# Kernel optimization log

Hardware: AMD Instinct MI355X
Metric: run time of the kernel (lower is better)

The kernel has to match this reference:

```python
import jax, jax.numpy as jnp
import numpy as np
import math

B, S, D, H = 4, 512, 1024, 16
DH = D // H
DQ = D // 4
MIN_STEPS, MAX_STEPS = 4, 12
THR = 1e-4


def lin(t, w, b):
    # torch Linear convention: w is (out, in)
    return jnp.einsum('...i,oi->...o', t, w) + b


def gelu(t):
    return jax.nn.gelu(t, approximate=False)  # torch nn.GELU() exact


def layernorm(t, g, b):
    m = t.mean(-1, keepdims=True)
    v = jnp.mean(jnp.square(t - m), axis=-1, keepdims=True)
    return (t - m) * jax.lax.rsqrt(v + 1e-5) * g + b


def _forward(h, x, ig_w1, ig_b1, ig_w2, ig_b2, wq, bq, wk, bk, wv, bv, wo, bo,
             g1_w1, g1_b1, g1_w2, g1_b2, gate_logits, ln_g, ln_b,
             sp_w1, sp_b1, sp_w2, sp_b2):
    # adaptive step count: steps = base + floor(sigmoid(MLP(mean_pool(h))).mean() * extra)
    pooled = h.mean(axis=1)  # (B, D)
    extra = jax.nn.sigmoid(lin(gelu(lin(pooled, sp_w1, sp_b1)), sp_w2, sp_b2)).mean()
    num_steps = jnp.minimum(
        MIN_STEPS + jnp.floor(extra * (MAX_STEPS - MIN_STEPS)).astype(jnp.int32), MAX_STEPS)

    gw = jax.nn.softmax(gate_logits)  # gate weights over the 3 gates
    scale = 1.0 / math.sqrt(DH)

    def step(carry, i):
        h, active = carry
        # G1 gate (G2/G3 multiply zero memory/expert outputs -> drop)
        G1 = jax.nn.sigmoid(lin(gelu(lin(h, g1_w1, g1_b1)), g1_w2, g1_b2)) * gw[0]
        # Phi: input-gated blend + raw multi-head self-attention
        gate = jax.nn.sigmoid(
            lin(gelu(lin(jnp.concatenate([h, x], axis=-1), ig_w1, ig_b1)), ig_w2, ig_b2))
        blended = gate * h + (1.0 - gate) * x
        q = lin(blended, wq, bq).reshape(B, S, H, DH)
        k = lin(blended, wk, bk).reshape(B, S, H, DH)
        v = lin(blended, wv, bv).reshape(B, S, H, DH)
        attn = jax.nn.softmax(jnp.einsum('bqhd,bkhd->bhqk', q, k) * scale, axis=-1)
        ctx = jnp.einsum('bhqk,bkhd->bqhd', attn, v).reshape(B, S, D)
        phi = lin(ctx, wo, bo)
        h_new = layernorm(h + G1 * phi, ln_g, ln_b)
        res = jnp.linalg.norm(h_new - h) / (jnp.linalg.norm(h) + 1e-8)
        act_i = active & (i < num_steps)
        h = jnp.where(act_i, h_new, h)
        active = act_i & jnp.logical_not((i >= MIN_STEPS) & (res < THR))
        return (h, active), None

    (h, _), _ = jax.lax.scan(step, (h, jnp.array(True)), jnp.arange(MAX_STEPS))
    return h


def setup_inputs() -> dict:
    key = jax.random.key(0)
    ks = jax.random.split(key, 16)
    f32 = jnp.float32

    def W(k, out_d, in_d):
        return jax.random.normal(k, (out_d, in_d), f32) * (1.0 / np.sqrt(in_d))

    return {
        'h': jax.random.normal(ks[0], (B, S, D), f32),
        'x': jax.random.normal(ks[1], (B, S, D), f32),
        # PhiLayer input_gate: Linear(2D, D/4) -> GELU -> Linear(D/4, D) -> Sigmoid
        'ig_w1': W(ks[2], DQ, 2 * D), 'ig_b1': jnp.zeros((DQ,), f32),
        'ig_w2': W(ks[3], D, DQ), 'ig_b2': jnp.zeros((D,), f32),
        # QKV / out projections (xavier-ish, zero bias)
        'wq': W(ks[4], D, D), 'bq': jnp.zeros((D,), f32),
        'wk': W(ks[5], D, D), 'bk': jnp.zeros((D,), f32),
        'wv': W(ks[6], D, D), 'bv': jnp.zeros((D,), f32),
        'wo': W(ks[7], D, D), 'bo': jnp.zeros((D,), f32),
        # Gating gate #1 MLP (only G1 contributes; memory/experts are zero)
        'g1_w1': W(ks[8], DQ, D), 'g1_b1': jnp.zeros((DQ,), f32),
        'g1_w2': W(ks[9], D, DQ), 'g1_b2': jnp.zeros((D,), f32),
        'gate_logits': jnp.ones((3,), f32),  # nn.Parameter(torch.ones(3))
        # LayerNorm
        'ln_g': jnp.ones((D,), f32), 'ln_b': jnp.zeros((D,), f32),
        # step predictor: Linear(D, D/4) -> GELU -> Linear(D/4, 1)
        'sp_w1': W(ks[10], DQ, D), 'sp_b1': jnp.zeros((DQ,), f32),
        'sp_w2': W(ks[11], 1, DQ), 'sp_b2': jnp.zeros((1,), f32),
    }


def reference(h, x, ig_w1, ig_b1, ig_w2, ig_b2, wq, bq, wk, bk, wv, bv, wo, bo,
              g1_w1, g1_b1, g1_w2, g1_b2, gate_logits, ln_g, ln_b,
              sp_w1, sp_b1, sp_w2, sp_b2):
    return _forward(h, x, ig_w1, ig_b1, ig_w2, ig_b2, wq, bq, wk, bk, wv, bv, wo, bo,
                    g1_w1, g1_b1, g1_w2, g1_b2, gate_logits, ln_g, ln_b,
                    sp_w1, sp_b1, sp_w2, sp_b2)
```

## Files before the change

### kernel.cpp

```cpp
#include <hip/hip_runtime.h>
#include <hip/hip_bf16.h>


#define B_   4
#define S_   512
#define D_   1024
#define H_   16
#define DH_  64
#define MSEQ 2048

typedef short short8 __attribute__((ext_vector_type(8)));
typedef float floatx4 __attribute__((ext_vector_type(4)));

static constexpr size_t OFF_H    = 0;
static constexpr size_t OFF_X    = 2097152;
static constexpr size_t OFF_HXB  = 4194304;
static constexpr size_t OFF_T2B  = 6291456;
static constexpr size_t OFF_T1B  = 6553600;
static constexpr size_t OFF_G1B  = 6815744;
static constexpr size_t OFF_QKVB = 7864320;
static constexpr size_t OFF_U    = 7864320;
static constexpr size_t OFF_CTXB = 11010048;
static constexpr size_t OFF_WARE = 12058624;
static constexpr size_t OFF_BIAS = 14811136;
static constexpr size_t OFF_POOL = 14817792;
static constexpr size_t OFF_SPT  = 14821888;
static constexpr size_t OFF_PPART= 14822912;
static constexpr size_t OFF_SCAL = 14888448;

static constexpr int W_WIG1 = 0;
static constexpr int W_WIG2 = 524288;
static constexpr int W_WG1  = 786432;
static constexpr int W_WG2  = 1048576;
static constexpr int W_QKV  = 1310720;
static constexpr int W_WO   = 4456448;
static constexpr int W_TOT  = 5505024;
static constexpr int B_TOT  = 6656;

__device__ __forceinline__ float bf2f(unsigned int u) {
  return __uint_as_float((u & 0xFFFFu) << 16);
}
__device__ __forceinline__ short f2bs(float f) {
  __hip_bfloat16 b = __float2bfloat16(f);
  return *reinterpret_cast<short*>(&b);
}
__device__ __forceinline__ unsigned int pk2(float lo, float hi) {
  return (unsigned int)(unsigned short)f2bs(lo) | ((unsigned int)(unsigned short)f2bs(hi) << 16);
}
__device__ __forceinline__ float ldf(const void* p, size_t i, int f32m) {
  return f32m ? ((const float*)p)[i] : bf2f(((const unsigned short*)p)[i]);
}
__device__ __forceinline__ float gelu_f(float x) {
  return 0.5f * x * (1.0f + erff(x * 0.70710678118654752440f));
}
__device__ __forceinline__ float sig_f(float x) {
  return 1.0f / (1.0f + expf(-x));
}
__device__ __forceinline__ void gl_lds16(const short* gp, short* lp) {
  __builtin_amdgcn_global_load_lds(
      (const __attribute__((address_space(1))) unsigned int*)gp,
      (__attribute__((address_space(3))) unsigned int*)lp, 16, 0, 0);
}
__device__ __forceinline__ float wave_sum(float v) {
  #pragma unroll
  for (int off = 32; off > 0; off >>= 1) v += __shfl_xor(v, off);
  return v;
}

__global__ void detect_kernel(const void* ln_g, int* dtf) {
  *dtf = (((const unsigned int*)ln_g)[0] == 0x3F800000u) ? 1 : 0;
}

struct RepackPtrs {
  const void* w[8];
  const void* b[8];
};

__global__ __launch_bounds__(256) void repack_all_kernel(
    const int* __restrict__ dtf, RepackPtrs ps,
    short* __restrict__ wdst, float* __restrict__ bdst) {
  const int f32m = *dtf;
  int i = blockIdx.x * 256 + threadIdx.x;
  if (i < W_TOT) {
    const int off[9] = {0, 524288, 786432, 1048576, 1310720, 2359296, 3407872, 4456448, W_TOT};
    int seg = 0;
    #pragma unroll
    for (int s = 1; s < 8; s++) seg += (i >= off[s]) ? 1 : 0;
    wdst[i] = f2bs(ldf(ps.w[seg], i - off[seg], f32m));
  } else if (i < W_TOT + B_TOT) {
    int j = i - W_TOT;
    const int off[9] = {0, 256, 1280, 1536, 2560, 3584, 4608, 5632, B_TOT};
    int seg = 0;
    #pragma unroll
    for (int s = 1; s < 8; s++) seg += (j >= off[s]) ? 1 : 0;
    bdst[j] = ldf(ps.b[seg], j - off[seg], f32m);
  }
}

__global__ __launch_bounds__(256) void cvt_in_kernel(
    const int* __restrict__ dtf, const void* __restrict__ hb,
    const void* __restrict__ xb, float* __restrict__ h, float* __restrict__ x,
    short* __restrict__ hxb, int n) {
  int f32m = *dtf;
  int i = blockIdx.x * 256 + threadIdx.x;
  if (i < n) {
    float hv = ldf(hb, i, f32m);
    float xv = ldf(xb, i, f32m);
    h[i] = hv;
    x[i] = xv;
    int row = i >> 10, col = i & 1023;
    hxb[(size_t)row * 2048 + col] = f2bs(hv);
    hxb[(size_t)row * 2048 + 1024 + col] = f2bs(xv);
  }
}

__global__ __launch_bounds__(256) void cvt_out_kernel(
    const int* __restrict__ dtf, const float* __restrict__ h, void* __restrict__ out, int n) {
  int f32m = *dtf;
  int i = blockIdx.x * 256 + threadIdx.x;
  if (i < n) {
    if (f32m) ((float*)out)[i] = h[i];
    else ((__hip_bfloat16*)out)[i] = __float2bfloat16(h[i]);
  }
}

__global__ __launch_bounds__(256) void pool_s1_kernel(
    const float* __restrict__ H, float* __restrict__ part) {
  int b = blockIdx.x, c = blockIdx.y, tid = threadIdx.x;
  const float* p = H + ((size_t)b * S_ + c * 32) * D_;
  #pragma unroll
  for (int rep = 0; rep < 4; rep++) {
    int d = rep * 256 + tid;
    float s = 0.f;
    for (int r = 0; r < 32; r++) s += p[(size_t)r * D_ + d];
    part[((size_t)b * 16 + c) * D_ + d] = s;
  }
}
__global__ __launch_bounds__(256) void pool_s2_kernel(
    const float* __restrict__ part, float* __restrict__ pooled) {
  int i = blockIdx.x * 256 + threadIdx.x;
  int b = i >> 10, d = i & 1023;
  float s = 0.f;
  #pragma unroll
  for (int c = 0; c < 16; c++) s += part[((size_t)b * 16 + c) * D_ + d];
  pooled[i] = s * (1.0f / (float)S_);
}

__device__ __forceinline__ float blk_sum256(float v, float* sm, int tid) {
  #pragma unroll
  for (int off = 32; off > 0; off >>= 1) v += __shfl_xor(v, off);
  __syncthreads();
  if ((tid & 63) == 0) sm[tid >> 6] = v;
  __syncthreads();
  return sm[0] + sm[1] + sm[2] + sm[3];
}

__global__ __launch_bounds__(256) void sp1_kernel(
    const int* __restrict__ dtf, const float* __restrict__ pooled,
    const void* __restrict__ w1, const void* __restrict__ b1,
    float* __restrict__ spt) {
  __shared__ float sm[4];
  const int f32m = *dtf;
  int j = blockIdx.x, tid = threadIdx.x;
  float s[4] = {0.f, 0.f, 0.f, 0.f};
  #pragma unroll
  for (int r = 0; r < 4; r++) {
    int k = tid * 4 + r;
    float w = ldf(w1, (size_t)j * D_ + k, f32m);
    s[0] += pooled[k] * w;
    s[1] += pooled[1024 + k] * w;
    s[2] += pooled[2048 + k] * w;
    s[3] += pooled[3072 + k] * w;
  }
  #pragma unroll
  for (int b = 0; b < 4; b++) {
    float t = blk_sum256(s[b], sm, tid);
    __syncthreads();
    if (tid == 0) spt[b * 256 + j] = gelu_f(t + ldf(b1, j, f32m));
  }
}

__global__ __launch_bounds__(256) void sp2_kernel(
    const int* __restrict__ dtf, const float* __restrict__ spt,
    const void* __restrict__ w2, const void* __restrict__ b2,
    const void* __restrict__ glog,
    int* __restrict__ num_steps, int* __restrict__ active, int* __restrict__ cur,
    float* __restrict__ gw0, float* __restrict__ ssd, float* __restrict__ ssh,
    int* __restrict__ cnt) {
  __shared__ float z[4];
  const int f32m = *dtf;
  int tid = threadIdx.x;
  if (tid < 12) cnt[tid] = 0;
  int wave = tid >> 6, lane = tid & 63;
  {
    int b = wave;
    float s = spt[b * 256 + lane]       * ldf(w2, lane, f32m) +
              spt[b * 256 + lane + 64]  * ldf(w2, lane + 64, f32m) +
              spt[b * 256 + lane + 128] * ldf(w2, lane + 128, f32m) +
              spt[b * 256 + lane + 192] * ldf(w2, lane + 192, f32m);
    #pragma unroll
    for (int off = 32; off > 0; off >>= 1) s += __shfl_xor(s, off);
    if (lane == 0) z[b] = sig_f(s + ldf(b2, 0, f32m));
  }
  __syncthreads();
  if (tid == 0) {
    float extra = 0.25f * (z[0] + z[1] + z[2] + z[3]);
    int ns = 4 + (int)floorf(extra * 8.0f);
    if (ns > 12) ns = 12;
    *num_steps = ns;
    *active = 1;
    *cur = 1;
    *ssd = 0.f; *ssh = 0.f;
    float g0 = ldf(glog, 0, f32m);
    float g1 = ldf(glog, 1, f32m);
    float g2 = ldf(glog, 2, f32m);
    float mx = fmaxf(g0, fmaxf(g1, g2));
    float e0 = expf(g0 - mx), e1 = expf(g1 - mx), e2 = expf(g2 - mx);
    *gw0 = e0 / (e0 + e1 + e2);
  }
}

enum { EPI_NONE = 0, EPI_GELU = 1, EPI_SIGSCALE = 2, EPI_BLEND = 3, EPI_RESADD = 4 };

template <int EPI, int BM, int BN>
__device__ __forceinline__ void mgemm_core(
    short* As, short* Bs,
    const short* __restrict__ A, int lda,
    const short* __restrict__ W, const float* __restrict__ bias, int K, int N,
    float* __restrict__ Cf, short* __restrict__ Cb,
    const float* __restrict__ aux1, const float* __restrict__ aux2f,
    const short* __restrict__ aux2b, const float* __restrict__ scale_ptr,
    int m0, int n0) {
  constexpr int FM = (BM / 2) / 16;
  constexpr int FN = (BN / 2) / 16;
  constexpr int CPA = (BM / 16) / 4;
  constexpr int CPB = (BN / 16) / 4;
  const int tid = threadIdx.x;
  const int lane = tid & 63, wv_ = tid >> 6;
  const int wm = (wv_ >> 1) * (BM / 2), wn = (wv_ & 1) * (BN / 2);
  const int srow = lane >> 2, scol = (lane & 3) * 8;
  const int frow = lane & 15, fk = (lane >> 4) * 8;

  floatx4 acc[FM][FN];
  #pragma unroll
  for (int i = 0; i < FM; i++)
    #pragma unroll
    for (int j = 0; j < FN; j++) acc[i][j] = (floatx4){0.f, 0.f, 0.f, 0.f};

  for (int k0 = 0; k0 < K; k0 += 64) {
    __syncthreads();
    #pragma unroll
    for (int c = 0; c < CPA; c++) {
      int q = wv_ * CPA + c;
      const short* gp = A + (size_t)(m0 + q * 16 + srow) * lda + k0 + scol;
      gl_lds16(gp, As + q * 512);
      gl_lds16(gp + 32, As + BM * 32 + q * 512);
    }
    #pragma unroll
    for (int c = 0; c < CPB; c++) {
      int q = wv_ * CPB + c;
      const short* gp = W + (size_t)(n0 + q * 16 + srow) * K + k0 + scol;
      gl_lds16(gp, Bs + q * 512);
      gl_lds16(gp + 32, Bs + BN * 32 + q * 512);
    }
    __syncthreads();
    #pragma unroll
    for (int hlf = 0; hlf < 2; hlf++) {
      const short* Ah = As + hlf * BM * 32;
      const short* Bh = Bs + hlf * BN * 32;
      short8 a[FM], b[FN];
      #pragma unroll
      for (int i = 0; i < FM; i++)
        a[i] = *reinterpret_cast<const short8*>(&Ah[(wm + i * 16 + frow) * 32 + fk]);
      #pragma unroll
      for (int j = 0; j < FN; j++)
        b[j] = *reinterpret_cast<const short8*>(&Bh[(wn + j * 16 + frow) * 32 + fk]);
      #pragma unroll
      for (int i = 0; i < FM; i++)
        #pragma unroll
        for (int j = 0; j < FN; j++)
          acc[i][j] = __builtin_amdgcn_mfma_f32_16x16x32_bf16(a[i], b[j], acc[i][j], 0, 0, 0);
    }
  }

  float gwv = 0.f;
  if (EPI == EPI_SIGSCALE) gwv = *scale_ptr;
  const int rq = (lane >> 4) * 4;
  #pragma unroll
  for (int i = 0; i < FM; i++) {
    #pragma unroll
    for (int j = 0; j < FN; j++) {
      int n = n0 + wn + j * 16 + (lane & 15);
      float bv = bias[n];
      #pragma unroll
      for (int r = 0; r < 4; r++) {
        int m = m0 + wm + i * 16 + rq + r;
        size_t off = (size_t)m * N + n;
        float v = acc[i][j][r] + bv;
        if (EPI == EPI_GELU) {
          Cb[off] = f2bs(gelu_f(v));
        } else if (EPI == EPI_SIGSCALE) {
          Cb[off] = f2bs(sig_f(v) * gwv);
        } else if (EPI == EPI_BLEND) {
          float s = sig_f(v);
          Cb[off] = f2bs(s * aux1[off] + (1.f - s) * aux2f[off]);
        } else if (EPI == EPI_RESADD) {
          Cf[off] = aux1[off] + bf2f((unsigned short)aux2b[off]) * v;
        } else {
          Cb[off] = f2bs(v);
        }
      }
    }
  }
}

template <int EPI, int BM, int BN>
__global__ __launch_bounds__(256) void mgemm(
    const int* __restrict__ flag, const short* __restrict__ A, int lda,
    const short* __restrict__ W, const float* __restrict__ bias, int K, int N,
    float* __restrict__ Cf, short* __restrict__ Cb,
    const float* __restrict__ aux1, const float* __restrict__ aux2f,
    const short* __restrict__ aux2b, const float* __restrict__ scale_ptr) {
  if (*flag == 0) return;
  __shared__ short As[BM * 64];
  __shared__ short Bs[BN * 64];
  mgemm_core<EPI, BM, BN>(As, Bs, A, lda, W, bias, K, N, Cf, Cb,
                          aux1, aux2f, aux2b, scale_ptr,
                          blockIdx.y * BM, blockIdx.x * BN);
}

__global__ __launch_bounds__(256) void gate1_kernel(
    const int* __restrict__ flag, const short* __restrict__ hxb,
    const short* __restrict__ warena, const float* __restrict__ biasA,
    short* __restrict__ t2b, short* __restrict__ t1b) {
  if (*flag == 0) return;
  __shared__ short As[64 * 64];
  __shared__ short Bs[64 * 64];
  if (blockIdx.z == 0)
    mgemm_core<EPI_GELU, 64, 64>(As, Bs, hxb, 2048, warena + W_WIG1, biasA + 0,
                                 2048, 256, nullptr, t2b, nullptr, nullptr, nullptr,
                                 nullptr, blockIdx.y * 64, blockIdx.x * 64);
  else
    mgemm_core<EPI_GELU, 64, 64>(As, Bs, hxb, 2048, warena + W_WG1, biasA + 1280,
                                 1024, 256, nullptr, t1b, nullptr, nullptr, nullptr,
                                 nullptr, blockIdx.y * 64, blockIdx.x * 64);
}

__global__ __launch_bounds__(256) void gate2_kernel(
    const int* __restrict__ flag, const short* __restrict__ t2b,
    const short* __restrict__ t1b, const short* __restrict__ warena,
    const float* __restrict__ biasA, short* __restrict__ bldb,
    short* __restrict__ g1b, const float* __restrict__ h,
    const float* __restrict__ xf, const float* __restrict__ gw0) {
  if (*flag == 0) return;
  __shared__ short As[128 * 64];
  __shared__ short Bs[64 * 64];
  if (blockIdx.z == 0)
    mgemm_core<EPI_BLEND, 128, 64>(As, Bs, t2b, 256, warena + W_WIG2, biasA + 256,
                                   256, 1024, nullptr, bldb, h, xf, nullptr,
                                   nullptr, blockIdx.y * 128, blockIdx.x * 64);
  else
    mgemm_core<EPI_SIGSCALE, 128, 64>(As, Bs, t1b, 256, warena + W_WG2, biasA + 1536,
                                      256, 1024, nullptr, g1b, nullptr, nullptr,
                                      nullptr, gw0, blockIdx.y * 128, blockIdx.x * 64);
}

#define AP_ 72
__global__ __launch_bounds__(256) void attn_kernel(
    const int* __restrict__ flag, const short* __restrict__ qkv,
    short* __restrict__ ctxb) {
  if (*flag == 0) return;
  __shared__ short Ks[64 * AP_];
  __shared__ short Vt[64 * AP_];
  __shared__ short Ps[64 * AP_];
  const int tid = threadIdx.x;
  const int lane = tid & 63, wv = tid >> 6;
  const int ln15 = lane & 15, quad = lane >> 4;
  const int qt = blockIdx.x, hh = blockIdx.y, b = blockIdx.z;
  const int wm = wv * 16;
  const size_t rowbase = (size_t)b * S_;
  const int hcol = hh * DH_;
  const float scale = 0.125f;

  short8 qa[2];
  {
    const short* qp = qkv + (rowbase + qt * 64 + wm + ln15) * 3072 + hcol + quad * 8;
    qa[0] = *reinterpret_cast<const short8*>(qp);
    qa[1] = *reinterpret_cast<const short8*>(qp + 32);
  }
  const int skk = tid >> 2, scg = (tid & 3) * 16;

  float mrow[4] = {-1e30f, -1e30f, -1e30f, -1e30f};
  float lrow[4] = {0.f, 0.f, 0.f, 0.f};
  floatx4 accO[4];
  #pragma unroll
  for (int j = 0; j < 4; j++) accO[j] = (floatx4){0.f, 0.f, 0.f, 0.f};

  for (int kt = 0; kt < 8; kt++) {
    __syncthreads();
    {
      const short* gk = qkv + (rowbase + kt * 64 + skk) * 3072 + 1024 + hcol + scg;
      uint4 k0 = *reinterpret_cast<const uint4*>(gk);
      uint4 k1 = *reinterpret_cast<const uint4*>(gk + 8);
      *reinterpret_cast<uint4*>(&Ks[skk * AP_ + scg]) = k0;
      *reinterpret_cast<uint4*>(&Ks[skk * AP_ + scg + 8]) = k1;
      short8 v0 = *reinterpret_cast<const short8*>(gk + 1024);
      short8 v1 = *reinterpret_cast<const short8*>(gk + 1032);
      #pragma unroll
      for (int j = 0; j < 8; j++) Vt[(scg + j) * AP_ + skk] = v0[j];
      #pragma unroll
      for (int j = 0; j < 8; j++) Vt[(scg + 8 + j) * AP_ + skk] = v1[j];
    }
    __syncthreads();

    floatx4 sc[4];
    #pragma unroll
    for (int nf = 0; nf < 4; nf++) {
      short8 b0 = *reinterpret_cast<const short8*>(&Ks[(nf * 16 + ln15) * AP_ + quad * 8]);
      short8 b1 = *reinterpret_cast<const short8*>(&Ks[(nf * 16 + ln15) * AP_ + 32 + quad * 8]);
      floatx4 s = (floatx4){0.f, 0.f, 0.f, 0.f};
      s = __builtin_amdgcn_mfma_f32_16x16x32_bf16(qa[0], b0, s, 0, 0, 0);
      s = __builtin_amdgcn_mfma_f32_16x16x32_bf16(qa[1], b1, s, 0, 0, 0);
      sc[nf] = s;
    }

    float prob[4][4];
    #pragma unroll
    for (int r = 0; r < 4; r++) {
      float lm = fmaxf(fmaxf(sc[0][r], sc[1][r]), fmaxf(sc[2][r], sc[3][r])) * scale;
      lm = fmaxf(lm, __shfl_xor(lm, 1));
      lm = fmaxf(lm, __shfl_xor(lm, 2));
      lm = fmaxf(lm, __shfl_xor(lm, 4));
      lm = fmaxf(lm, __shfl_xor(lm, 8));
      float mn = fmaxf(mrow[r], lm);
      float alpha = expf(mrow[r] - mn);
      float ls = 0.f;
      #pragma unroll
      for (int nf = 0; nf < 4; nf++) {
        float p = expf(sc[nf][r] * scale - mn);
        prob[nf][r] = p;
        ls += p;
      }
      ls += __shfl_xor(ls, 1);
      ls += __shfl_xor(ls, 2);
      ls += __shfl_xor(ls, 4);
      ls += __shfl_xor(ls, 8);
      lrow[r] = lrow[r] * alpha + ls;
      mrow[r] = mn;
      #pragma unroll
      for (int df = 0; df < 4; df++) accO[df][r] *= alpha;
    }
    #pragma unroll
    for (int nf = 0; nf < 4; nf++)
      #pragma unroll
      for (int r = 0; r < 4; r++)
        Ps[(wm + quad * 4 + r) * AP_ + nf * 16 + ln15] = f2bs(prob[nf][r]);
    __syncthreads();

    short8 pa0 = *reinterpret_cast<const short8*>(&Ps[(wm + ln15) * AP_ + quad * 8]);
    short8 pa1 = *reinterpret_cast<const short8*>(&Ps[(wm + ln15) * AP_ + 32 + quad * 8]);
    #pragma unroll
    for (int df = 0; df < 4; df++) {
      short8 bv0 = *reinterpret_cast<const short8*>(&Vt[(df * 16 + ln15) * AP_ + quad * 8]);
      short8 bv1 = *reinterpret_cast<const short8*>(&Vt[(df * 16 + ln15) * AP_ + 32 + quad * 8]);
      accO[df] = __builtin_amdgcn_mfma_f32_16x16x32_bf16(pa0, bv0, accO[df], 0, 0, 0);
      accO[df] = __builtin_amdgcn_mfma_f32_16x16x32_bf16(pa1, bv1, accO[df], 0, 0, 0);
    }
  }

  float inv[4];
  #pragma unroll
  for (int r = 0; r < 4; r++) inv[r] = 1.0f / lrow[r];
  #pragma unroll
  for (int df = 0; df < 4; df++) {
    #pragma unroll
    for (int r = 0; r < 4; r++) {
      size_t off = (rowbase + qt * 64 + wm + quad * 4 + r) * 1024 + hcol + df * 16 + ln15;
      ctxb[off] = f2bs(accO[df][r] * inv[r]);
    }
  }
}

__global__ __launch_bounds__(256) void ln_kernel(
    int step_i, const int* __restrict__ flagp, const int* __restrict__ dtf,
    const float* __restrict__ U, float* __restrict__ H, short* __restrict__ hxb,
    const void* __restrict__ g, const void* __restrict__ be,
    float* __restrict__ ssd, float* __restrict__ ssh,
    int* __restrict__ active, int* __restrict__ cur,
    const int* __restrict__ num_steps, int* __restrict__ cnt) {
  const int flag = *flagp;
  const int f32m = *dtf;
  __shared__ float sdd[4], sdh[4];
  const int tid = threadIdx.x;
  const int wv = tid >> 6, lane = tid & 63;
  if (flag) {
    const int row = blockIdx.x * 4 + wv;
    const float4* u4 = reinterpret_cast<const float4*>(U + (size_t)row * D_);
    float4* h4 = reinterpret_cast<float4*>(H + (size_t)row * D_);
    float4 uv[4], hv[4];
    #pragma unroll
    for (int j = 0; j < 4; j++) uv[j] = u4[lane + 64 * j];
    #pragma unroll
    for (int j = 0; j < 4; j++) hv[j] = h4[lane + 64 * j];
    float s = 0.f;
    #pragma unroll
    for (int j = 0; j < 4; j++) s += (uv[j].x + uv[j].y) + (uv[j].z + uv[j].w);
    s = wave_sum(s);
    float mean = s * (1.0f / (float)D_);
    float4 d[4];
    float vv = 0.f;
    #pragma unroll
    for (int j = 0; j < 4; j++) {
      d[j].x = uv[j].x - mean; d[j].y = uv[j].y - mean;
      d[j].z = uv[j].z - mean; d[j].w = uv[j].w - mean;
      vv += d[j].x * d[j].x + d[j].y * d[j].y + d[j].z * d[j].z + d[j].w * d[j].w;
    }
    vv = wave_sum(vv);
    float rstd = rsqrtf(vv * (1.0f / (float)D_) + 1e-5f);
    float lsd = 0.f, lsh = 0.f;
    #pragma unroll
    for (int j = 0; j < 4; j++) {
      int c = (lane + 64 * j) * 4;
      float hn0 = d[j].x * rstd * ldf(g, c + 0, f32m) + ldf(be, c + 0, f32m);
      float hn1 = d[j].y * rstd * ldf(g, c + 1, f32m) + ldf(be, c + 1, f32m);
      float hn2 = d[j].z * rstd * ldf(g, c + 2, f32m) + ldf(be, c + 2, f32m);
      float hn3 = d[j].w * rstd * ldf(g, c + 3, f32m) + ldf(be, c + 3, f32m);
      float e0 = hn0 - hv[j].x, e1 = hn1 - hv[j].y, e2 = hn2 - hv[j].z, e3 = hn3 - hv[j].w;
      lsd += e0 * e0 + e1 * e1 + e2 * e2 + e3 * e3;
      lsh += hv[j].x * hv[j].x + hv[j].y * hv[j].y + hv[j].z * hv[j].z + hv[j].w * hv[j].w;
      h4[lane + 64 * j] = make_float4(hn0, hn1, hn2, hn3);
      uint2 pw;
      pw.x = pk2(hn0, hn1);
      pw.y = pk2(hn2, hn3);
      *reinterpret_cast<uint2*>(hxb + (size_t)row * 2048 + c) = pw;
    }
    lsd = wave_sum(lsd);
    lsh = wave_sum(lsh);
    if (lane == 0) { sdd[wv] = lsd; sdh[wv] = lsh; }
    __syncthreads();
    if (tid == 0) {
      atomicAdd(ssd, (sdd[0] + sdd[1]) + (sdd[2] + sdd[3]));
      atomicAdd(ssh, (sdh[0] + sdh[1]) + (sdh[2] + sdh[3]));
    }
  }
  if (tid == 0) {
    __threadfence();
    int old = atomicAdd(&cnt[step_i], 1);
    if (old == (int)gridDim.x - 1) {
      if (flag && step_i >= 4) {
        float nd = atomicAdd(ssd, 0.0f);
        float nh = atomicAdd(ssh, 0.0f);
        float res = sqrtf(nd) / (sqrtf(nh) + 1e-8f);
        if (res < 1e-4f) *active = 0;
      }
      *cur = ((*active) && (step_i + 1 < *num_steps)) ? 1 : 0;
      *ssd = 0.f; *ssh = 0.f;
    }
  }
}

extern "C" void kernel_launch(void* const* d_in, const int* in_sizes, int n_in,
                              void* d_out, int out_size, void* d_ws, size_t ws_size,
                              hipStream_t stream) {
  (void)in_sizes; (void)n_in; (void)out_size; (void)ws_size;
  const void* h_in  = d_in[0];
  const void* x_in  = d_in[1];
  const void* glog  = d_in[18];
  const void* ln_g  = d_in[19];
  const void* ln_b  = d_in[20];
  const void* sp_w1 = d_in[21];
  const void* sp_b1 = d_in[22];
  const void* sp_w2 = d_in[23];
  const void* sp_b2 = d_in[24];

  RepackPtrs rp;
  rp.w[0] = d_in[2];  rp.w[1] = d_in[4];  rp.w[2] = d_in[14]; rp.w[3] = d_in[16];
  rp.w[4] = d_in[6];  rp.w[5] = d_in[8];  rp.w[6] = d_in[10]; rp.w[7] = d_in[12];
  rp.b[0] = d_in[3];  rp.b[1] = d_in[5];  rp.b[2] = d_in[15]; rp.b[3] = d_in[17];
  rp.b[4] = d_in[7];  rp.b[5] = d_in[9];  rp.b[6] = d_in[11]; rp.b[7] = d_in[13];

  float* wsf = (float*)d_ws;
  float* h      = wsf + OFF_H;
  float* xf     = wsf + OFF_X;
  short* hxb    = (short*)(wsf + OFF_HXB);
  short* t2b    = (short*)(wsf + OFF_T2B);
  short* t1b    = (short*)(wsf + OFF_T1B);
  short* g1b    = (short*)(wsf + OFF_G1B);
  short* qkvb   = (short*)(wsf + OFF_QKVB);
  float* u      = wsf + OFF_U;
  short* ctxb   = (short*)(wsf + OFF_CTXB);
  short* bldb   = ctxb;
  short* warena = (short*)(wsf + OFF_WARE);
  float* biasA  = wsf + OFF_BIAS;
  float* pooled = wsf + OFF_POOL;
  float* spt    = wsf + OFF_SPT;
  float* ppart  = wsf + OFF_PPART;
  float* ssd    = wsf + OFF_SCAL + 0;
  float* ssh    = wsf + OFF_SCAL + 1;
  float* gw0    = wsf + OFF_SCAL + 2;
  int* ip        = (int*)(wsf + OFF_SCAL + 8);
  int* num_steps = ip + 0;
  int* active    = ip + 1;
  int* cur       = ip + 2;
  int* dtf       = ip + 3;
  int* cnt       = ip + 4;

  const int NTOT = B_ * S_ * D_;

  detect_kernel<<<1, 1, 0, stream>>>(ln_g, dtf);
  repack_all_kernel<<<(W_TOT + B_TOT + 255) / 256, 256, 0, stream>>>(dtf, rp, warena, biasA);
  cvt_in_kernel<<<NTOT / 256, 256, 0, stream>>>(dtf, h_in, x_in, h, xf, hxb, NTOT);
  pool_s1_kernel<<<dim3(4, 16), 256, 0, stream>>>(h, ppart);
  pool_s2_kernel<<<16, 256, 0, stream>>>(ppart, pooled);
  sp1_kernel<<<256, 256, 0, stream>>>(dtf, pooled, sp_w1, sp_b1, spt);
  sp2_kernel<<<1, 256, 0, stream>>>(dtf, spt, sp_w2, sp_b2, glog,
                                    num_steps, active, cur, gw0, ssd, ssh, cnt);
  for (int i = 0; i < 12; i++) {
    gate1_kernel<<<dim3(4, 32, 2), 256, 0, stream>>>(cur, hxb, warena, biasA, t2b, t1b);
    gate2_kernel<<<dim3(16, 16, 2), 256, 0, stream>>>(cur, t2b, t1b, warena, biasA,
                                                      bldb, g1b, h, xf, gw0);
    mgemm<EPI_NONE, 128, 64><<<dim3(48, 16), 256, 0, stream>>>(
        cur, bldb, 1024, warena + W_QKV, biasA + 2560, 1024, 3072,
        nullptr, qkvb, nullptr, nullptr, nullptr, nullptr);
    attn_kernel<<<dim3(8, 16, 4), 256, 0, stream>>>(cur, qkvb, ctxb);
    mgemm<EPI_RESADD, 64, 64><<<dim3(16, 32), 256, 0, stream>>>(
        cur, ctxb, 1024, warena + W_WO, biasA + 5632, 1024, 1024,
        u, nullptr, h, nullptr, g1b, nullptr);
    ln_kernel<<<512, 256, 0, stream>>>(i, cur, dtf, u, h, hxb, ln_g, ln_b,
                                       ssd, ssh, active, cur, num_steps, cnt);
  }
  cvt_out_kernel<<<NTOT / 256, 256, 0, stream>>>(dtf, h, (void*)d_out, NTOT);
}
```

Before: 1.236 ms.

## Fuse per-step kernels into one cooperative kernel with grid syncs

Replaces the six kernel launches per iteration (two gate GEMM stages, QKV GEMM, attention, output GEMM, layernorm) with one cooperative kernel of 512 blocks that runs each stage as a persistent tile loop separated by grid.sync(). This removes five launch boundaries per step and the repeated flag checks. In exchange, the grid is fixed at 512 blocks, so the 768-tile QKV stage needs a second pass on some blocks, and grid-wide barriers add their own cost. A shared 27KB LDS buffer is reused across stages.

```diff
diff --git a/kernel.cpp b/kernel.cpp
--- a/kernel.cpp
+++ b/kernel.cpp
@@ -1,5 +1,8 @@
 #include <hip/hip_runtime.h>
 #include <hip/hip_bf16.h>
+#include <hip/hip_cooperative_groups.h>
+
+namespace cg = cooperative_groups;
 
 
 #define B_   4
@@ -8,6 +11,7 @@
 #define H_   16
 #define DH_  64
 #define MSEQ 2048
+#define GRID_ 512
 
 typedef short short8 __attribute__((ext_vector_type(8)));
 typedef float floatx4 __attribute__((ext_vector_type(4)));
@@ -314,69 +318,17 @@
   }
 }
 
-template <int EPI, int BM, int BN>
-__global__ __launch_bounds__(256) void mgemm(
-    const int* __restrict__ flag, const short* __restrict__ A, int lda,
-    const short* __restrict__ W, const float* __restrict__ bias, int K, int N,
-    float* __restrict__ Cf, short* __restrict__ Cb,
-    const float* __restrict__ aux1, const float* __restrict__ aux2f,
-    const short* __restrict__ aux2b, const float* __restrict__ scale_ptr) {
-  if (*flag == 0) return;
-  __shared__ short As[BM * 64];
-  __shared__ short Bs[BN * 64];
-  mgemm_core<EPI, BM, BN>(As, Bs, A, lda, W, bias, K, N, Cf, Cb,
-                          aux1, aux2f, aux2b, scale_ptr,
-                          blockIdx.y * BM, blockIdx.x * BN);
-}
-
-__global__ __launch_bounds__(256) void gate1_kernel(
-    const int* __restrict__ flag, const short* __restrict__ hxb,
-    const short* __restrict__ warena, const float* __restrict__ biasA,
-    short* __restrict__ t2b, short* __restrict__ t1b) {
-  if (*flag == 0) return;
-  __shared__ short As[64 * 64];
-  __shared__ short Bs[64 * 64];
-  if (blockIdx.z == 0)
-    mgemm_core<EPI_GELU, 64, 64>(As, Bs, hxb, 2048, warena + W_WIG1, biasA + 0,
-                                 2048, 256, nullptr, t2b, nullptr, nullptr, nullptr,
-                                 nullptr, blockIdx.y * 64, blockIdx.x * 64);
-  else
-    mgemm_core<EPI_GELU, 64, 64>(As, Bs, hxb, 2048, warena + W_WG1, biasA + 1280,
-                                 1024, 256, nullptr, t1b, nullptr, nullptr, nullptr,
-                                 nullptr, blockIdx.y * 64, blockIdx.x * 64);
-}
-
-__global__ __launch_bounds__(256) void gate2_kernel(
-    const int* __restrict__ flag, const short* __restrict__ t2b,
-    const short* __restrict__ t1b, const short* __restrict__ warena,
-    const float* __restrict__ biasA, short* __restrict__ bldb,
-    short* __restrict__ g1b, const float* __restrict__ h,
-    const float* __restrict__ xf, const float* __restrict__ gw0) {
-  if (*flag == 0) return;
-  __shared__ short As[128 * 64];
-  __shared__ short Bs[64 * 64];
-  if (blockIdx.z == 0)
-    mgemm_core<EPI_BLEND, 128, 64>(As, Bs, t2b, 256, warena + W_WIG2, biasA + 256,
-                                   256, 1024, nullptr, bldb, h, xf, nullptr,
-                                   nullptr, blockIdx.y * 128, blockIdx.x * 64);
-  else
-    mgemm_core<EPI_SIGSCALE, 128, 64>(As, Bs, t1b, 256, warena + W_WG2, biasA + 1536,
-                                      256, 1024, nullptr, g1b, nullptr, nullptr,
-                                      nullptr, gw0, blockIdx.y * 128, blockIdx.x * 64);
-}
-
 #define AP_ 72
-__global__ __launch_bounds__(256) void attn_kernel(
-    const int* __restrict__ flag, const short* __restrict__ qkv,
-    short* __restrict__ ctxb) {
-  if (*flag == 0) return;
-  __shared__ short Ks[64 * AP_];
-  __shared__ short Vt[64 * AP_];
-  __shared__ short Ps[64 * AP_];
+__device__ __forceinline__ void attn_phase(
+    int t, const short* __restrict__ qkv, short* __restrict__ ctxb,
+    short* __restrict__ smem) {
+  short* Ks = smem;
+  short* Vt = smem + 64 * AP_;
+  short* Ps = smem + 128 * AP_;
   const int tid = threadIdx.x;
   const int lane = tid & 63, wv = tid >> 6;
   const int ln15 = lane & 15, quad = lane >> 4;
-  const int qt = blockIdx.x, hh = blockIdx.y, b = blockIdx.z;
+  const int qt = t & 7, hh = (t >> 3) & 15, b = t >> 7;
   const int wm = wv * 16;
   const size_t rowbase = (size_t)b * S_;
   const int hcol = hh * DH_;
@@ -481,73 +433,68 @@
   }
 }
 
-__global__ __launch_bounds__(256) void ln_kernel(
-    int step_i, const int* __restrict__ flagp, const int* __restrict__ dtf,
+__device__ __forceinline__ void ln_phase(
+    int step_i, const int* __restrict__ dtf,
     const float* __restrict__ U, float* __restrict__ H, short* __restrict__ hxb,
     const void* __restrict__ g, const void* __restrict__ be,
     float* __restrict__ ssd, float* __restrict__ ssh,
     int* __restrict__ active, int* __restrict__ cur,
-    const int* __restrict__ num_steps, int* __restrict__ cnt) {
-  const int flag = *flagp;
+    const int* __restrict__ num_steps, int* __restrict__ cnt, int bid) {
   const int f32m = *dtf;
   __shared__ float sdd[4], sdh[4];
   const int tid = threadIdx.x;
   const int wv = tid >> 6, lane = tid & 63;
-  if (flag) {
-    const int row = blockIdx.x * 4 + wv;
-    const float4* u4 = reinterpret_cast<const float4*>(U + (size_t)row * D_);
-    float4* h4 = reinterpret_cast<float4*>(H + (size_t)row * D_);
-    float4 uv[4], hv[4];
-    #pragma unroll
-    for (int j = 0; j < 4; j++) uv[j] = u4[lane + 64 * j];
-    #pragma unroll
-    for (int j = 0; j < 4; j++) hv[j] = h4[lane + 64 * j];
-    float s = 0.f;
-    #pragma unroll
-    for (int j = 0; j < 4; j++) s += (uv[j].x + uv[j].y) + (uv[j].z + uv[j].w);
-    s = wave_sum(s);
-    float mean = s * (1.0f / (float)D_);
-    float4 d[4];
-    float vv = 0.f;
-    #pragma unroll
-    for (int j = 0; j < 4; j++) {
-      d[j].x = uv[j].x - mean; d[j].y = uv[j].y - mean;
-      d[j].z = uv[j].z - mean; d[j].w = uv[j].w - mean;
-      vv += d[j].x * d[j].x + d[j].y * d[j].y + d[j].z * d[j].z + d[j].w * d[j].w;
-    }
-    vv = wave_sum(vv);
-    float rstd = rsqrtf(vv * (1.0f / (float)D_) + 1e-5f);
-    float lsd = 0.f, lsh = 0.f;
-    #pragma unroll
-    for (int j = 0; j < 4; j++) {
-      int c = (lane + 64 * j) * 4;
-      float hn0 = d[j].x * rstd * ldf(g, c + 0, f32m) + ldf(be, c + 0, f32m);
-      float hn1 = d[j].y * rstd * ldf(g, c + 1, f32m) + ldf(be, c + 1, f32m);
-      float hn2 = d[j].z * rstd * ldf(g, c + 2, f32m) + ldf(be, c + 2, f32m);
-      float hn3 = d[j].w * rstd * ldf(g, c + 3, f32m) + ldf(be, c + 3, f32m);
-      float e0 = hn0 - hv[j].x, e1 = hn1 - hv[j].y, e2 = hn2 - hv[j].z, e3 = hn3 - hv[j].w;
-      lsd += e0 * e0 + e1 * e1 + e2 * e2 + e3 * e3;
-      lsh += hv[j].x * hv[j].x + hv[j].y * hv[j].y + hv[j].z * hv[j].z + hv[j].w * hv[j].w;
-      h4[lane + 64 * j] = make_float4(hn0, hn1, hn2, hn3);
-      uint2 pw;
-      pw.x = pk2(hn0, hn1);
-      pw.y = pk2(hn2, hn3);
-      *reinterpret_cast<uint2*>(hxb + (size_t)row * 2048 + c) = pw;
-    }
-    lsd = wave_sum(lsd);
-    lsh = wave_sum(lsh);
-    if (lane == 0) { sdd[wv] = lsd; sdh[wv] = lsh; }
-    __syncthreads();
-    if (tid == 0) {
-      atomicAdd(ssd, (sdd[0] + sdd[1]) + (sdd[2] + sdd[3]));
-      atomicAdd(ssh, (sdh[0] + sdh[1]) + (sdh[2] + sdh[3]));
-    }
-  }
+  const int row = bid * 4 + wv;
+  const float4* u4 = reinterpret_cast<const float4*>(U + (size_t)row * D_);
+  float4* h4 = reinterpret_cast<float4*>(H + (size_t)row * D_);
+  float4 uv[4], hv[4];
+  #pragma unroll
+  for (int j = 0; j < 4; j++) uv[j] = u4[lane + 64 * j];
+  #pragma unroll
+  for (int j = 0; j < 4; j++) hv[j] = h4[lane + 64 * j];
+  float s = 0.f;
+  #pragma unroll
+  for (int j = 0; j < 4; j++) s += (uv[j].x + uv[j].y) + (uv[j].z + uv[j].w);
+  s = wave_sum(s);
+  float mean = s * (1.0f / (float)D_);
+  float4 d[4];
+  float vv = 0.f;
+  #pragma unroll
+  for (int j = 0; j < 4; j++) {
+    d[j].x = uv[j].x - mean; d[j].y = uv[j].y - mean;
+    d[j].z = uv[j].z - mean; d[j].w = uv[j].w - mean;
+    vv += d[j].x * d[j].x + d[j].y * d[j].y + d[j].z * d[j].z + d[j].w * d[j].w;
+  }
+  vv = wave_sum(vv);
+  float rstd = rsqrtf(vv * (1.0f / (float)D_) + 1e-5f);
+  float lsd = 0.f, lsh = 0.f;
+  #pragma unroll
+  for (int j = 0; j < 4; j++) {
+    int c = (lane + 64 * j) * 4;
+    float hn0 = d[j].x * rstd * ldf(g, c + 0, f32m) + ldf(be, c + 0, f32m);
+    float hn1 = d[j].y * rstd * ldf(g, c + 1, f32m) + ldf(be, c + 1, f32m);
+    float hn2 = d[j].z * rstd * ldf(g, c + 2, f32m) + ldf(be, c + 2, f32m);
+    float hn3 = d[j].w * rstd * ldf(g, c + 3, f32m) + ldf(be, c + 3, f32m);
+    float e0 = hn0 - hv[j].x, e1 = hn1 - hv[j].y, e2 = hn2 - hv[j].z, e3 = hn3 - hv[j].w;
+    lsd += e0 * e0 + e1 * e1 + e2 * e2 + e3 * e3;
+    lsh += hv[j].x * hv[j].x + hv[j].y * hv[j].y + hv[j].z * hv[j].z + hv[j].w * hv[j].w;
+    h4[lane + 64 * j] = make_float4(hn0, hn1, hn2, hn3);
+    uint2 pw;
+    pw.x = pk2(hn0, hn1);
+    pw.y = pk2(hn2, hn3);
+    *reinterpret_cast<uint2*>(hxb + (size_t)row * 2048 + c) = pw;
+  }
+  lsd = wave_sum(lsd);
+  lsh = wave_sum(lsh);
+  if (lane == 0) { sdd[wv] = lsd; sdh[wv] = lsh; }
+  __syncthreads();
   if (tid == 0) {
+    atomicAdd(ssd, (sdd[0] + sdd[1]) + (sdd[2] + sdd[3]));
+    atomicAdd(ssh, (sdh[0] + sdh[1]) + (sdh[2] + sdh[3]));
     __threadfence();
     int old = atomicAdd(&cnt[step_i], 1);
-    if (old == (int)gridDim.x - 1) {
-      if (flag && step_i >= 4) {
+    if (old == GRID_ - 1) {
+      if (step_i >= 4) {
         float nd = atomicAdd(ssd, 0.0f);
         float nh = atomicAdd(ssh, 0.0f);
         float res = sqrtf(nd) / (sqrtf(nh) + 1e-8f);
@@ -557,6 +504,91 @@
       *ssd = 0.f; *ssh = 0.f;
     }
   }
+}
+
+struct StepArgs {
+  int step_i;
+  const int* cur_r;
+  const int* dtf;
+  short* hxb;
+  short* t2b;
+  short* t1b;
+  short* bldb;
+  short* g1b;
+  short* qkvb;
+  short* ctxb;
+  float* u;
+  const short* warena;
+  const float* biasA;
+  float* h;
+  const float* xf;
+  const float* gw0;
+  const void* ln_g;
+  const void* ln_b;
+  float* ssd;
+  float* ssh;
+  int* active;
+  int* cur_w;
+  const int* num_steps;
+  int* cnt;
+};
+
+__global__ __launch_bounds__(256, 2) void step_kernel(StepArgs a) {
+  if (*a.cur_r == 0) return;
+  cg::grid_group grid = cg::this_grid();
+  __shared__ short smem[13824];
+  const int bid = blockIdx.x;
+
+  for (int t = bid; t < 256; t += GRID_) {
+    int z = t >> 7, r = t & 127;
+    int n0 = (r & 3) * 64, m0 = (r >> 2) * 64;
+    if (z == 0)
+      mgemm_core<EPI_GELU, 64, 64>(smem, smem + 64 * 64, a.hxb, 2048,
+                                   a.warena + W_WIG1, a.biasA + 0, 2048, 256,
+                                   nullptr, a.t2b, nullptr, nullptr, nullptr, nullptr, m0, n0);
+    else
+      mgemm_core<EPI_GELU, 64, 64>(smem, smem + 64 * 64, a.hxb, 2048,
+                                   a.warena + W_WG1, a.biasA + 1280, 1024, 256,
+                                   nullptr, a.t1b, nullptr, nullptr, nullptr, nullptr, m0, n0);
+  }
+  grid.sync();
+
+  for (int t = bid; t < 512; t += GRID_) {
+    int z = t >> 8, r = t & 255;
+    int n0 = (r & 15) * 64, m0 = (r >> 4) * 128;
+    if (z == 0)
+      mgemm_core<EPI_BLEND, 128, 64>(smem, smem + 128 * 64, a.t2b, 256,
+                                     a.warena + W_WIG2, a.biasA + 256, 256, 1024,
+                                     nullptr, a.bldb, a.h, a.xf, nullptr, nullptr, m0, n0);
+    else
+      mgemm_core<EPI_SIGSCALE, 128, 64>(smem, smem + 128 * 64, a.t1b, 256,
+                                        a.warena + W_WG2, a.biasA + 1536, 256, 1024,
+                                        nullptr, a.g1b, nullptr, nullptr, nullptr, a.gw0, m0, n0);
+  }
+  grid.sync();
+
+  for (int t = bid; t < 768; t += GRID_) {
+    int n0 = (t % 48) * 64, m0 = (t / 48) * 128;
+    mgemm_core<EPI_NONE, 128, 64>(smem, smem + 128 * 64, a.bldb, 1024,
+                                  a.warena + W_QKV, a.biasA + 2560, 1024, 3072,
+                                  nullptr, a.qkvb, nullptr, nullptr, nullptr, nullptr, m0, n0);
+  }
+  grid.sync();
+
+  for (int t = bid; t < 512; t += GRID_)
+    attn_phase(t, a.qkvb, a.ctxb, smem);
+  grid.sync();
+
+  for (int t = bid; t < 512; t += GRID_) {
+    int n0 = (t & 15) * 64, m0 = (t >> 4) * 64;
+    mgemm_core<EPI_RESADD, 64, 64>(smem, smem + 64 * 64, a.ctxb, 1024,
+                                   a.warena + W_WO, a.biasA + 5632, 1024, 1024,
+                                   a.u, nullptr, a.h, nullptr, a.g1b, nullptr, m0, n0);
+  }
+  grid.sync();
+
+  ln_phase(a.step_i, a.dtf, a.u, a.h, a.hxb, a.ln_g, a.ln_b,
+           a.ssd, a.ssh, a.active, a.cur_w, a.num_steps, a.cnt, bid);
 }
 
 extern "C" void kernel_launch(void* const* d_in, const int* in_sizes, int n_in,
@@ -615,19 +647,24 @@
   sp1_kernel<<<256, 256, 0, stream>>>(dtf, pooled, sp_w1, sp_b1, spt);
   sp2_kernel<<<1, 256, 0, stream>>>(dtf, spt, sp_w2, sp_b2, glog,
                                     num_steps, active, cur, gw0, ssd, ssh, cnt);
+
   for (int i = 0; i < 12; i++) {
-    gate1_kernel<<<dim3(4, 32, 2), 256, 0, stream>>>(cur, hxb, warena, biasA, t2b, t1b);
-    gate2_kernel<<<dim3(16, 16, 2), 256, 0, stream>>>(cur, t2b, t1b, warena, biasA,
-                                                      bldb, g1b, h, xf, gw0);
-    mgemm<EPI_NONE, 128, 64><<<dim3(48, 16), 256, 0, stream>>>(
-        cur, bldb, 1024, warena + W_QKV, biasA + 2560, 1024, 3072,
-        nullptr, qkvb, nullptr, nullptr, nullptr, nullptr);
-    attn_kernel<<<dim3(8, 16, 4), 256, 0, stream>>>(cur, qkvb, ctxb);
-    mgemm<EPI_RESADD, 64, 64><<<dim3(16, 32), 256, 0, stream>>>(
-        cur, ctxb, 1024, warena + W_WO, biasA + 5632, 1024, 1024,
-        u, nullptr, h, nullptr, g1b, nullptr);
-    ln_kernel<<<512, 256, 0, stream>>>(i, cur, dtf, u, h, hxb, ln_g, ln_b,
-                                       ssd, ssh, active, cur, num_steps, cnt);
-  }
+    StepArgs sa;
+    sa.step_i = i;
+    sa.cur_r = cur;      sa.dtf = dtf;
+    sa.hxb = hxb;        sa.t2b = t2b;    sa.t1b = t1b;
+    sa.bldb = bldb;      sa.g1b = g1b;
+    sa.qkvb = qkvb;      sa.ctxb = ctxb;  sa.u = u;
+    sa.warena = warena;  sa.biasA = biasA;
+    sa.h = h;            sa.xf = xf;      sa.gw0 = gw0;
+    sa.ln_g = ln_g;      sa.ln_b = ln_b;
+    sa.ssd = ssd;        sa.ssh = ssh;
+    sa.active = active;  sa.cur_w = cur;
+    sa.num_steps = num_steps;             sa.cnt = cnt;
+    void* ka[1] = { (void*)&sa };
+    hipLaunchCooperativeKernel(reinterpret_cast<void*>(step_kernel),
+                               dim3(GRID_), dim3(256), ka, 0, stream);
+  }
+
   cvt_out_kernel<<<NTOT / 256, 256, 0, stream>>>(dtf, h, (void*)d_out, NTOT);
 }
```

After: 3.635 ms. 2.94x slower.

## Fuse gate GEMM stages and Wo GEMM with LayerNorm using inter-block counters

Applied to the files above, without the earlier changes.

The two gate-MLP GEMM kernels are merged into one launch. Second-stage blocks spin on per-row-band atomic counters until the first-stage tiles they depend on are written. The Wo projection GEMM and the LayerNorm/residual-check kernel are also merged: each block finishes its GEMM tile, waits on a band counter until all 16 tiles of its 64-row band are done, then normalizes 4 rows. This cuts two launches and grid-wide barriers per step and lets dependent work start early, but it relies on producer blocks being resident or scheduled ahead of spinning consumers.

```diff
diff --git a/kernel.cpp b/kernel.cpp
--- a/kernel.cpp
+++ b/kernel.cpp
@@ -8,6 +8,7 @@
 #define H_   16
 #define DH_  64
 #define MSEQ 2048
+#define GRID_ 512
 
 typedef short short8 __attribute__((ext_vector_type(8)));
 typedef float floatx4 __attribute__((ext_vector_type(4)));
@@ -190,7 +191,7 @@
   __shared__ float z[4];
   const int f32m = *dtf;
   int tid = threadIdx.x;
-  if (tid < 12) cnt[tid] = 0;
+  for (int zz = tid; zz < 784; zz += 256) cnt[zz] = 0;
   int wave = tid >> 6, lane = tid & 63;
   {
     int b = wave;
@@ -329,40 +330,50 @@
                           blockIdx.y * BM, blockIdx.x * BN);
 }
 
-__global__ __launch_bounds__(256) void gate1_kernel(
-    const int* __restrict__ flag, const short* __restrict__ hxb,
-    const short* __restrict__ warena, const float* __restrict__ biasA,
-    short* __restrict__ t2b, short* __restrict__ t1b) {
-  if (*flag == 0) return;
-  __shared__ short As[64 * 64];
-  __shared__ short Bs[64 * 64];
-  if (blockIdx.z == 0)
-    mgemm_core<EPI_GELU, 64, 64>(As, Bs, hxb, 2048, warena + W_WIG1, biasA + 0,
-                                 2048, 256, nullptr, t2b, nullptr, nullptr, nullptr,
-                                 nullptr, blockIdx.y * 64, blockIdx.x * 64);
-  else
-    mgemm_core<EPI_GELU, 64, 64>(As, Bs, hxb, 2048, warena + W_WG1, biasA + 1280,
-                                 1024, 256, nullptr, t1b, nullptr, nullptr, nullptr,
-                                 nullptr, blockIdx.y * 64, blockIdx.x * 64);
-}
-
-__global__ __launch_bounds__(256) void gate2_kernel(
-    const int* __restrict__ flag, const short* __restrict__ t2b,
-    const short* __restrict__ t1b, const short* __restrict__ warena,
-    const float* __restrict__ biasA, short* __restrict__ bldb,
-    short* __restrict__ g1b, const float* __restrict__ h,
-    const float* __restrict__ xf, const float* __restrict__ gw0) {
-  if (*flag == 0) return;
+__global__ __launch_bounds__(256) void gate12_kernel(
+    int step_i, const int* __restrict__ flagp,
+    const short* __restrict__ hxb, const short* __restrict__ warena,
+    const float* __restrict__ biasA, short* __restrict__ t2b,
+    short* __restrict__ t1b, short* __restrict__ bldb, short* __restrict__ g1b,
+    const float* __restrict__ h, const float* __restrict__ xf,
+    const float* __restrict__ gw0, int* __restrict__ gcnt) {
+  if (*flagp == 0) return;
   __shared__ short As[128 * 64];
   __shared__ short Bs[64 * 64];
-  if (blockIdx.z == 0)
-    mgemm_core<EPI_BLEND, 128, 64>(As, Bs, t2b, 256, warena + W_WIG2, biasA + 256,
-                                   256, 1024, nullptr, bldb, h, xf, nullptr,
-                                   nullptr, blockIdx.y * 128, blockIdx.x * 64);
-  else
-    mgemm_core<EPI_SIGSCALE, 128, 64>(As, Bs, t1b, 256, warena + W_WG2, biasA + 1536,
-                                      256, 1024, nullptr, g1b, nullptr, nullptr,
-                                      nullptr, gw0, blockIdx.y * 128, blockIdx.x * 64);
+  const int id = blockIdx.x;
+  int* gc = gcnt + step_i * 32;
+  if (id < 256) {
+    int z = id >> 7, r = id & 127;
+    int n0 = (r & 3) * 64, m0 = (r >> 2) * 64;
+    if (z == 0)
+      mgemm_core<EPI_GELU, 64, 64>(As, Bs, hxb, 2048, warena + W_WIG1, biasA + 0,
+                                   2048, 256, nullptr, t2b, nullptr, nullptr,
+                                   nullptr, nullptr, m0, n0);
+    else
+      mgemm_core<EPI_GELU, 64, 64>(As, Bs, hxb, 2048, warena + W_WG1, biasA + 1280,
+                                   1024, 256, nullptr, t1b, nullptr, nullptr,
+                                   nullptr, nullptr, m0, n0);
+    __threadfence();
+    __syncthreads();
+    if (threadIdx.x == 0) atomicAdd(&gc[z * 16 + (r >> 3)], 1);
+  } else {
+    int r = id - 256;
+    int z = r >> 8, rr = r & 255;
+    int n0 = (rr & 15) * 64, m0 = (rr >> 4) * 128;
+    if (threadIdx.x == 0) {
+      while (atomicAdd(&gc[z * 16 + (rr >> 4)], 0) < 8) __builtin_amdgcn_s_sleep(8);
+      __threadfence();
+    }
+    __syncthreads();
+    if (z == 0)
+      mgemm_core<EPI_BLEND, 128, 64>(As, Bs, t2b, 256, warena + W_WIG2, biasA + 256,
+                                     256, 1024, nullptr, bldb, h, xf, nullptr,
+                                     nullptr, m0, n0);
+    else
+      mgemm_core<EPI_SIGSCALE, 128, 64>(As, Bs, t1b, 256, warena + W_WG2, biasA + 1536,
+                                        256, 1024, nullptr, g1b, nullptr, nullptr,
+                                        nullptr, gw0, m0, n0);
+  }
 }
 
 #define AP_ 72
@@ -481,73 +492,68 @@
   }
 }
 
-__global__ __launch_bounds__(256) void ln_kernel(
-    int step_i, const int* __restrict__ flagp, const int* __restrict__ dtf,
+__device__ __forceinline__ void ln_phase(
+    int step_i, const int* __restrict__ dtf,
     const float* __restrict__ U, float* __restrict__ H, short* __restrict__ hxb,
     const void* __restrict__ g, const void* __restrict__ be,
     float* __restrict__ ssd, float* __restrict__ ssh,
     int* __restrict__ active, int* __restrict__ cur,
-    const int* __restrict__ num_steps, int* __restrict__ cnt) {
-  const int flag = *flagp;
+    const int* __restrict__ num_steps, int* __restrict__ cnt, int bid) {
   const int f32m = *dtf;
   __shared__ float sdd[4], sdh[4];
   const int tid = threadIdx.x;
   const int wv = tid >> 6, lane = tid & 63;
-  if (flag) {
-    const int row = blockIdx.x * 4 + wv;
-    const float4* u4 = reinterpret_cast<const float4*>(U + (size_t)row * D_);
-    float4* h4 = reinterpret_cast<float4*>(H + (size_t)row * D_);
-    float4 uv[4], hv[4];
-    #pragma unroll
-    for (int j = 0; j < 4; j++) uv[j] = u4[lane + 64 * j];
-    #pragma unroll
-    for (int j = 0; j < 4; j++) hv[j] = h4[lane + 64 * j];
-    float s = 0.f;
-    #pragma unroll
-    for (int j = 0; j < 4; j++) s += (uv[j].x + uv[j].y) + (uv[j].z + uv[j].w);
-    s = wave_sum(s);
-    float mean = s * (1.0f / (float)D_);
-    float4 d[4];
-    float vv = 0.f;
-    #pragma unroll
-    for (int j = 0; j < 4; j++) {
-      d[j].x = uv[j].x - mean; d[j].y = uv[j].y - mean;
-      d[j].z = uv[j].z - mean; d[j].w = uv[j].w - mean;
-      vv += d[j].x * d[j].x + d[j].y * d[j].y + d[j].z * d[j].z + d[j].w * d[j].w;
-    }
-    vv = wave_sum(vv);
-    float rstd = rsqrtf(vv * (1.0f / (float)D_) + 1e-5f);
-    float lsd = 0.f, lsh = 0.f;
-    #pragma unroll
-    for (int j = 0; j < 4; j++) {
-      int c = (lane + 64 * j) * 4;
-      float hn0 = d[j].x * rstd * ldf(g, c + 0, f32m) + ldf(be, c + 0, f32m);
-      float hn1 = d[j].y * rstd * ldf(g, c + 1, f32m) + ldf(be, c + 1, f32m);
-      float hn2 = d[j].z * rstd * ldf(g, c + 2, f32m) + ldf(be, c + 2, f32m);
-      float hn3 = d[j].w * rstd * ldf(g, c + 3, f32m) + ldf(be, c + 3, f32m);
-      float e0 = hn0 - hv[j].x, e1 = hn1 - hv[j].y, e2 = hn2 - hv[j].z, e3 = hn3 - hv[j].w;
-      lsd += e0 * e0 + e1 * e1 + e2 * e2 + e3 * e3;
-      lsh += hv[j].x * hv[j].x + hv[j].y * hv[j].y + hv[j].z * hv[j].z + hv[j].w * hv[j].w;
-      h4[lane + 64 * j] = make_float4(hn0, hn1, hn2, hn3);
-      uint2 pw;
-      pw.x = pk2(hn0, hn1);
-      pw.y = pk2(hn2, hn3);
-      *reinterpret_cast<uint2*>(hxb + (size_t)row * 2048 + c) = pw;
-    }
-    lsd = wave_sum(lsd);
-    lsh = wave_sum(lsh);
-    if (lane == 0) { sdd[wv] = lsd; sdh[wv] = lsh; }
-    __syncthreads();
-    if (tid == 0) {
-      atomicAdd(ssd, (sdd[0] + sdd[1]) + (sdd[2] + sdd[3]));
-      atomicAdd(ssh, (sdh[0] + sdh[1]) + (sdh[2] + sdh[3]));
-    }
-  }
+  const int row = bid * 4 + wv;
+  const float4* u4 = reinterpret_cast<const float4*>(U + (size_t)row * D_);
+  float4* h4 = reinterpret_cast<float4*>(H + (size_t)row * D_);
+  float4 uv[4], hv[4];
+  #pragma unroll
+  for (int j = 0; j < 4; j++) uv[j] = u4[lane + 64 * j];
+  #pragma unroll
+  for (int j = 0; j < 4; j++) hv[j] = h4[lane + 64 * j];
+  float s = 0.f;
+  #pragma unroll
+  for (int j = 0; j < 4; j++) s += (uv[j].x + uv[j].y) + (uv[j].z + uv[j].w);
+  s = wave_sum(s);
+  float mean = s * (1.0f / (float)D_);
+  float4 d[4];
+  float vv = 0.f;
+  #pragma unroll
+  for (int j = 0; j < 4; j++) {
+    d[j].x = uv[j].x - mean; d[j].y = uv[j].y - mean;
+    d[j].z = uv[j].z - mean; d[j].w = uv[j].w - mean;
+    vv += d[j].x * d[j].x + d[j].y * d[j].y + d[j].z * d[j].z + d[j].w * d[j].w;
+  }
+  vv = wave_sum(vv);
+  float rstd = rsqrtf(vv * (1.0f / (float)D_) + 1e-5f);
+  float lsd = 0.f, lsh = 0.f;
+  #pragma unroll
+  for (int j = 0; j < 4; j++) {
+    int c = (lane + 64 * j) * 4;
+    float hn0 = d[j].x * rstd * ldf(g, c + 0, f32m) + ldf(be, c + 0, f32m);
+    float hn1 = d[j].y * rstd * ldf(g, c + 1, f32m) + ldf(be, c + 1, f32m);
+    float hn2 = d[j].z * rstd * ldf(g, c + 2, f32m) + ldf(be, c + 2, f32m);
+    float hn3 = d[j].w * rstd * ldf(g, c + 3, f32m) + ldf(be, c + 3, f32m);
+    float e0 = hn0 - hv[j].x, e1 = hn1 - hv[j].y, e2 = hn2 - hv[j].z, e3 = hn3 - hv[j].w;
+    lsd += e0 * e0 + e1 * e1 + e2 * e2 + e3 * e3;
+    lsh += hv[j].x * hv[j].x + hv[j].y * hv[j].y + hv[j].z * hv[j].z + hv[j].w * hv[j].w;
+    h4[lane + 64 * j] = make_float4(hn0, hn1, hn2, hn3);
+    uint2 pw;
+    pw.x = pk2(hn0, hn1);
+    pw.y = pk2(hn2, hn3);
+    *reinterpret_cast<uint2*>(hxb + (size_t)row * 2048 + c) = pw;
+  }
+  lsd = wave_sum(lsd);
+  lsh = wave_sum(lsh);
+  if (lane == 0) { sdd[wv] = lsd; sdh[wv] = lsh; }
+  __syncthreads();
   if (tid == 0) {
+    atomicAdd(ssd, (sdd[0] + sdd[1]) + (sdd[2] + sdd[3]));
+    atomicAdd(ssh, (sdh[0] + sdh[1]) + (sdh[2] + sdh[3]));
     __threadfence();
     int old = atomicAdd(&cnt[step_i], 1);
-    if (old == (int)gridDim.x - 1) {
-      if (flag && step_i >= 4) {
+    if (old == GRID_ - 1) {
+      if (step_i >= 4) {
         float nd = atomicAdd(ssd, 0.0f);
         float nh = atomicAdd(ssh, 0.0f);
         float res = sqrtf(nd) / (sqrtf(nh) + 1e-8f);
@@ -557,6 +563,36 @@
       *ssd = 0.f; *ssh = 0.f;
     }
   }
+}
+
+__global__ __launch_bounds__(256) void wo_ln_kernel(
+    int step_i, const int* __restrict__ flagp, const int* __restrict__ dtf,
+    const short* __restrict__ ctxb, const short* __restrict__ warena,
+    const float* __restrict__ biasA, float* __restrict__ u,
+    const short* __restrict__ g1b, float* __restrict__ h,
+    short* __restrict__ hxb, const void* __restrict__ ln_g,
+    const void* __restrict__ ln_b, float* __restrict__ ssd,
+    float* __restrict__ ssh, int* __restrict__ active, int* __restrict__ cur,
+    const int* __restrict__ num_steps, int* __restrict__ cnt,
+    int* __restrict__ bandcnt) {
+  if (*flagp == 0) return;
+  __shared__ short As[64 * 64];
+  __shared__ short Bs[64 * 64];
+  const int bx = blockIdx.x, by = blockIdx.y;
+  mgemm_core<EPI_RESADD, 64, 64>(As, Bs, ctxb, 1024, warena + W_WO, biasA + 5632,
+                                 1024, 1024, u, nullptr, h, nullptr, g1b, nullptr,
+                                 by * 64, bx * 64);
+  __threadfence();
+  __syncthreads();
+  int* bc = &bandcnt[step_i * 32 + by];
+  if (threadIdx.x == 0) {
+    atomicAdd(bc, 1);
+    while (atomicAdd(bc, 0) < 16) __builtin_amdgcn_s_sleep(8);
+    __threadfence();
+  }
+  __syncthreads();
+  ln_phase(step_i, dtf, u, h, hxb, ln_g, ln_b, ssd, ssh, active, cur,
+           num_steps, cnt, by * 16 + bx);
 }
 
 extern "C" void kernel_launch(void* const* d_in, const int* in_sizes, int n_in,
@@ -604,6 +640,8 @@
   int* cur       = ip + 2;
   int* dtf       = ip + 3;
   int* cnt       = ip + 4;
+  int* bandcnt   = ip + 16;
+  int* gcnt      = ip + 400;
 
   const int NTOT = B_ * S_ * D_;
 
@@ -615,19 +653,18 @@
   sp1_kernel<<<256, 256, 0, stream>>>(dtf, pooled, sp_w1, sp_b1, spt);
   sp2_kernel<<<1, 256, 0, stream>>>(dtf, spt, sp_w2, sp_b2, glog,
                                     num_steps, active, cur, gw0, ssd, ssh, cnt);
+
   for (int i = 0; i < 12; i++) {
-    gate1_kernel<<<dim3(4, 32, 2), 256, 0, stream>>>(cur, hxb, warena, biasA, t2b, t1b);
-    gate2_kernel<<<dim3(16, 16, 2), 256, 0, stream>>>(cur, t2b, t1b, warena, biasA,
-                                                      bldb, g1b, h, xf, gw0);
+    gate12_kernel<<<768, 256, 0, stream>>>(i, cur, hxb, warena, biasA,
+                                           t2b, t1b, bldb, g1b, h, xf, gw0, gcnt);
     mgemm<EPI_NONE, 128, 64><<<dim3(48, 16), 256, 0, stream>>>(
         cur, bldb, 1024, warena + W_QKV, biasA + 2560, 1024, 3072,
         nullptr, qkvb, nullptr, nullptr, nullptr, nullptr);
     attn_kernel<<<dim3(8, 16, 4), 256, 0, stream>>>(cur, qkvb, ctxb);
-    mgemm<EPI_RESADD, 64, 64><<<dim3(16, 32), 256, 0, stream>>>(
-        cur, ctxb, 1024, warena + W_WO, biasA + 5632, 1024, 1024,
-        u, nullptr, h, nullptr, g1b, nullptr);
-    ln_kernel<<<512, 256, 0, stream>>>(i, cur, dtf, u, h, hxb, ln_g, ln_b,
-                                       ssd, ssh, active, cur, num_steps, cnt);
-  }
+    wo_ln_kernel<<<dim3(16, 32), 256, 0, stream>>>(
+        i, cur, dtf, ctxb, warena, biasA, u, g1b, h, hxb, ln_g, ln_b,
+        ssd, ssh, active, cur, num_steps, cnt, bandcnt);
+  }
+
   cvt_out_kernel<<<NTOT / 256, 256, 0, stream>>>(dtf, h, (void*)d_out, NTOT);
 }
```

After: 2.280 ms. 1.84x slower.
